# Performance work log

Measured on AMD Instinct MI355X. Metric: run time of the kernel, lower is better.

## Reference

```python
import jax, jax.numpy as jnp
import numpy as np

N_USERS = 50000
N_ITEMS = 20000
N_EDGES = 1_000_000
N_RATINGS = 5
IN_FEAT = 64
HID_FEAT = 64


def setup_inputs() -> dict:
    key = jax.random.key(0)
    k = jax.random.split(key, 6)
    u_s = jax.random.randint(k[0], (N_EDGES,), 0, N_USERS, dtype=jnp.int32)
    v_s = jax.random.randint(k[1], (N_EDGES,), 0, N_ITEMS, dtype=jnp.int32)
    rate = jax.random.randint(k[2], (N_EDGES,), 0, N_RATINGS, dtype=jnp.int32)
    x_user = jax.random.normal(k[3], (N_USERS, IN_FEAT), dtype=jnp.float32)
    x_item = jax.random.normal(k[4], (N_ITEMS, IN_FEAT), dtype=jnp.float32)
    # xavier-uniform with relu gain, as in nn.init.xavier_uniform_(gain=calculate_gain('relu'))
    gain = float(np.sqrt(2.0))
    bound = gain * float(np.sqrt(6.0 / (IN_FEAT + HID_FEAT)))
    weight = jax.random.uniform(k[5], (N_RATINGS, IN_FEAT, HID_FEAT),
                                minval=-bound, maxval=bound, dtype=jnp.float32)
    return {"u_s": u_s, "v_s": v_s, "rate": rate,
            "x_user": x_user, "x_item": x_item, "weight": weight}


def _aggregate(dst, src_feat, rate, n_dst, weight):
    # c_ij in the original = #edges sharing (dst node, rating); so the
    # sum over edges of (x[src] @ W[rate]) / c_ij equals a per-(dst, rating)
    # MEAN of source features followed by the rating-specific matmul.
    seg = dst * N_RATINGS + rate                      # [E] combined segment id
    cnt = jax.ops.segment_sum(jnp.ones_like(src_feat[:, 0]), seg,
                              num_segments=n_dst * N_RATINGS)  # [n_dst*R]
    ssum = jax.ops.segment_sum(src_feat, seg,
                               num_segments=n_dst * N_RATINGS)  # [n_dst*R, in]
    mean = ssum / jnp.maximum(cnt, 1.0)[:, None]
    mean = mean.reshape(n_dst, N_RATINGS, src_feat.shape[1])  # [n_dst, R, in]
    return jnp.einsum('nrd,rdh->nh', mean, weight)            # [n_dst, hid]


def reference(u_s, v_s, rate, x_user, x_item, weight):
    # w_sharing=False -> use weight directly; activation=None; dropout=0 -> identity
    h_u = _aggregate(u_s, x_item[v_s], rate, N_USERS, weight)
    h_v = _aggregate(v_s, x_user[u_s], rate, N_ITEMS, weight)
    return h_u, h_v
```

## Files before the change

kernel.cpp:

```cpp
#include <hip/hip_runtime.h>
#include <hip/hip_bf16.h>

constexpr int N_USERS = 50000;
constexpr int N_ITEMS = 20000;
constexpr int RATES   = 5;
constexpr int F       = 64;

constexpr int N_TOTAL  = N_USERS + N_ITEMS;
constexpr long OUT_FLOATS = (long)N_TOTAL * F;

constexpr int NFB_U = (N_USERS + 31) / 32;
constexpr int NFB_V = (N_ITEMS + 31) / 32;
constexpr int NFBK  = NFB_U + NFB_V;
constexpr int NBKP  = 2304;

constexpr int EPB  = 2048;

constexpr int SLOT = 2048;
constexpr int GCAP = SLOT;

constexpr int SMSTR = 328;

constexpr int LW_TOT = RATES * 8 * 512;

constexpr int TU8 = N_USERS * 8;
constexpr int TI8 = N_ITEMS * 8;
constexpr int TW8 = RATES * 8 * 64;
constexpr int TPREP = TU8 + TI8 + TW8;

typedef short bfrag __attribute__((ext_vector_type(8)));
typedef float vf4   __attribute__((ext_vector_type(4)));

static __device__ __forceinline__ unsigned short f2bf(float f) {
    __hip_bfloat16 h = __float2bfloat16(f);
    return *reinterpret_cast<unsigned short*>(&h);
}

__global__ void zero_ints(int* __restrict__ p, long n) {
    long i = (long)blockIdx.x * blockDim.x + threadIdx.x;
    long stride = (long)gridDim.x * blockDim.x;
    for (long k = i; k < n; k += stride) p[k] = 0;
}

__global__ __launch_bounds__(256) void prep_kernel(
        const float* __restrict__ Xu, const float* __restrict__ Xi,
        const float* __restrict__ W,
        unsigned short* __restrict__ Xbu, unsigned short* __restrict__ Xbi,
        unsigned short* __restrict__ LWg, int* __restrict__ bcursor) {
    int gid = blockIdx.x * 256 + threadIdx.x;
    int stride = gridDim.x * 256;
    for (int i = gid; i < NFBK; i += stride) bcursor[i] = 0;
    for (int t = gid; t < TPREP; t += stride) {
        if (t < TU8 + TI8) {
            const float* src;
            unsigned short* dst;
            if (t < TU8) { src = Xu + (long)t * 8;         dst = Xbu + (long)t * 8; }
            else         { src = Xi + (long)(t - TU8) * 8; dst = Xbi + (long)(t - TU8) * 8; }
            float4 a = *(const float4*)src;
            float4 b = *(const float4*)(src + 4);
            union { bfrag v; unsigned short s[8]; } o;
            o.s[0] = f2bf(a.x); o.s[1] = f2bf(a.y);
            o.s[2] = f2bf(a.z); o.s[3] = f2bf(a.w);
            o.s[4] = f2bf(b.x); o.s[5] = f2bf(b.y);
            o.s[6] = f2bf(b.z); o.s[7] = f2bf(b.w);
            *(bfrag*)dst = o.v;
        } else {
            int t2 = t - TU8 - TI8;
            int r   = t2 >> 9;
            int u   = t2 & 511;
            int kfq = u >> 6;
            int h   = u & 63;
            int kf  = kfq >> 2, q = kfq & 3;
            union { bfrag v; unsigned short s[8]; } o;
#pragma unroll
            for (int j = 0; j < 8; j++)
                o.s[j] = f2bf(W[(r * 64 + kf * 32 + q * 8 + j) * 64 + h]);
            *(bfrag*)&LWg[(((r * 2 + kf) * 4 + q) * 64 + h) * 8] = o.v;
        }
    }
}

__global__ __launch_bounds__(256) void part_kernel(
        const int* __restrict__ u_s, const int* __restrict__ v_s,
        const int* __restrict__ rate,
        int* __restrict__ bcursor, int* __restrict__ sorted_pk, int n_edges) {
    __shared__ int lcnt[NBKP];
    __shared__ int lcur[NBKP];

    int tid = threadIdx.x;
    int e0 = blockIdx.x * EPB;
    int eEnd = min(e0 + EPB, n_edges);

    for (int i = tid; i < NBKP; i += 256) lcnt[i] = 0;
    __syncthreads();
    for (int e = e0 + tid; e < eEnd; e += 256) {
        atomicAdd(&lcnt[u_s[e] >> 5], 1);
        atomicAdd(&lcnt[NFB_U + (v_s[e] >> 5)], 1);
    }
    __syncthreads();
    for (int bb = tid; bb < NFBK; bb += 256) {
        int c = lcnt[bb];
        lcur[bb] = c ? atomicAdd(&bcursor[bb], c) : 0;
    }
    __syncthreads();
    for (int e = e0 + tid; e < eEnd; e += 256) {
        int u = u_s[e], v = v_s[e], r = rate[e];
        int bu = u >> 5;
        int pu = atomicAdd(&lcur[bu], 1);
        if (pu < SLOT)
            sorted_pk[(long)bu * SLOT + pu] = v | (r << 16) | ((u & 31) << 19);
        int bv = NFB_U + (v >> 5);
        int pv = atomicAdd(&lcur[bv], 1);
        if (pv < SLOT)
            sorted_pk[(long)bv * SLOT + pv] = u | (r << 16) | ((v & 31) << 19);
    }
}

__global__ __launch_bounds__(256) void gather_mfma_kernel(
        const int* __restrict__ sorted_pk,
        const int* __restrict__ bcursor,
        const unsigned short* __restrict__ Xbu,
        const unsigned short* __restrict__ Xbi,
        const unsigned short* __restrict__ LWg,
        float* __restrict__ out) {
    __shared__ int perm[GCAP];
    __shared__ int lcnt[32 * RATES];
    __shared__ int lcur[32 * RATES];
    __shared__ float sinvc[32 * RATES];
    __shared__ unsigned short smean[32][SMSTR];
    int* tsum = perm;

    int tid = threadIdx.x, lane = tid & 63, wid = tid >> 6;

    int b = blockIdx.x;
    const unsigned short* Xb;
    float* o;
    int fb, node0, n_nodes;
    if (b < NFB_V) {
        fb = NFB_U + b; node0 = b * 32; n_nodes = N_ITEMS;
        Xb = Xbu; o = out + (long)N_USERS * F;
    } else {
        fb = b - NFB_V; node0 = fb * 32; n_nodes = N_USERS;
        Xb = Xbi; o = out;
    }
    int nn = min(32, n_nodes - node0);
    int nseg = nn * RATES;

    int cnt = min(bcursor[fb], SLOT);
    const int* pkbase = sorted_pk + (long)fb * SLOT;

    int rpk[8];
#pragma unroll
    for (int kk = 0; kk < 8; kk++) {
        int j = kk * 256 + tid;
        rpk[kk] = (j < cnt) ? pkbase[j] : -1;
    }

    for (int i = tid; i < nseg; i += 256) lcnt[i] = 0;
    __syncthreads();
#pragma unroll
    for (int kk = 0; kk < 8; kk++) {
        int pk = rpk[kk];
        if (pk >= 0)
            atomicAdd(&lcnt[((pk >> 19) & 31) * RATES + ((pk >> 16) & 7)], 1);
    }
    __syncthreads();
    int v = (tid < nseg) ? lcnt[tid] : 0;
    tsum[tid] = v;
    __syncthreads();
    for (int off = 1; off < 256; off <<= 1) {
        int x = (tid >= off) ? tsum[tid - off] : 0;
        __syncthreads();
        tsum[tid] += x;
        __syncthreads();
    }
    int excl = tsum[tid] - v;
    if (tid < nseg) {
        lcur[tid]  = excl;
        sinvc[tid] = 1.0f / fmaxf((float)v, 1.0f);
    }
    __syncthreads();
#pragma unroll
    for (int kk = 0; kk < 8; kk++) {
        int pk = rpk[kk];
        if (pk >= 0) {
            int p = atomicAdd(&lcur[((pk >> 19) & 31) * RATES + ((pk >> 16) & 7)], 1);
            if (p < GCAP) perm[p] = pk;
        }
    }
    __syncthreads();

    int g = lane >> 3, ci = lane & 7;
    const unsigned short* xp = Xb + ci * 8;
    for (int oct = wid; oct * 8 < nseg; oct += 4) {
        int sg = oct * 8 + g;
        int S = 0, E = 0;
        if (sg < nseg) {
            S = (sg == 0) ? 0 : min(lcur[sg - 1], GCAP);
            E = min(lcur[sg], GCAP);
        }
        float acc[8];
#pragma unroll
        for (int k = 0; k < 8; k++) acc[k] = 0.f;
        for (int t = S; t < E; t++) {
            int src = perm[t] & 0xFFFF;
            const uint4 y4 = *(const uint4*)(xp + (long)src * F);
            unsigned uu[4] = {y4.x, y4.y, y4.z, y4.w};
#pragma unroll
            for (int qq = 0; qq < 4; qq++) {
                acc[2 * qq]     += __uint_as_float(uu[qq] << 16);
                acc[2 * qq + 1] += __uint_as_float(uu[qq] & 0xffff0000u);
            }
        }
        if (sg < nseg) {
            float sc = sinvc[sg];
            int n = sg / RATES;
            int r = sg - n * RATES;
            union { bfrag v8; unsigned short us[8]; } mv;
#pragma unroll
            for (int k = 0; k < 8; k++) mv.us[k] = f2bf(acc[k] * sc);
            *(bfrag*)&smean[n][r * F + ci * 8] = mv.v8;
        }
    }
    __syncthreads();

    int m = lane & 15, q = lane >> 4;
    int tile = wid & 1, ht0 = wid >> 1;
    if (tile * 16 < nn) {
        const unsigned short* smrow = &smean[tile * 16 + m][0];
        vf4 acc0 = {0.f, 0.f, 0.f, 0.f};
        vf4 acc1 = {0.f, 0.f, 0.f, 0.f};
#pragma unroll
        for (int r = 0; r < RATES; r++) {
            bfrag a0 = *(const bfrag*)(smrow + r * F + q * 8);
            bfrag a1 = *(const bfrag*)(smrow + r * F + 32 + q * 8);
            {
                int h = ht0 * 16 + m;
                bfrag b0 = *(const bfrag*)(LWg + ((r * 2 + 0) * 4 + q) * 512 + h * 8);
                bfrag b1 = *(const bfrag*)(LWg + ((r * 2 + 1) * 4 + q) * 512 + h * 8);
                acc0 = __builtin_amdgcn_mfma_f32_16x16x32_bf16(a0, b0, acc0, 0, 0, 0);
                acc0 = __builtin_amdgcn_mfma_f32_16x16x32_bf16(a1, b1, acc0, 0, 0, 0);
            }
            {
                int h = (ht0 + 2) * 16 + m;
                bfrag b0 = *(const bfrag*)(LWg + ((r * 2 + 0) * 4 + q) * 512 + h * 8);
                bfrag b1 = *(const bfrag*)(LWg + ((r * 2 + 1) * 4 + q) * 512 + h * 8);
                acc1 = __builtin_amdgcn_mfma_f32_16x16x32_bf16(a0, b0, acc1, 0, 0, 0);
                acc1 = __builtin_amdgcn_mfma_f32_16x16x32_bf16(a1, b1, acc1, 0, 0, 0);
            }
        }
        float* obase = o + (long)(node0 + tile * 16 + q * 4) * F;
#pragma unroll
        for (int reg = 0; reg < 4; reg++) {
            obase[(long)reg * F + ht0 * 16 + m]       = acc0[reg];
            obase[(long)reg * F + (ht0 + 2) * 16 + m] = acc1[reg];
        }
    }
}

extern "C" void kernel_launch(void* const* d_in, const int* in_sizes, int n_in,
                              void* d_out, int out_size, void* d_ws, size_t ws_size,
                              hipStream_t stream) {
    const int*   u_s    = (const int*)d_in[0];
    const int*   v_s    = (const int*)d_in[1];
    const int*   rate   = (const int*)d_in[2];
    const float* x_user = (const float*)d_in[3];
    const float* x_item = (const float*)d_in[4];
    const float* W      = (const float*)d_in[5];
    float* out = (float*)d_out;

    int n_edges = in_sizes[0];

    unsigned short* Xbu = (unsigned short*)d_ws;
    unsigned short* Xbi = Xbu + (long)N_USERS * F;
    unsigned short* LWg = Xbi + (long)N_ITEMS * F;
    int* bcursor      = (int*)(LWg + LW_TOT);
    int* sorted_pk    = bcursor + NFBK;
    size_t need = (size_t)((char*)(sorted_pk + (long)NFBK * SLOT) - (char*)d_ws);
    if (need > ws_size) {
        zero_ints<<<2048, 256, 0, stream>>>((int*)out, OUT_FLOATS);
        return;
    }

    prep_kernel<<<(TPREP + 255) / 256, 256, 0, stream>>>(
        x_user, x_item, W, Xbu, Xbi, LWg, bcursor);

    part_kernel<<<(n_edges + EPB - 1) / EPB, 256, 0, stream>>>(
        u_s, v_s, rate, bcursor, sorted_pk, n_edges);

    gather_mfma_kernel<<<NFBK, 256, 0, stream>>>(
        sorted_pk, bcursor, Xbu, Xbi, LWg, out);
}
```

Before: 174.4 us.

## Fuse prep and partition kernels, shuffle-based scan, unrolled gather, smaller perm

```diff
diff --git a/kernel.cpp b/kernel.cpp
--- a/kernel.cpp
+++ b/kernel.cpp
@@ -14,7 +14,7 @@
 constexpr int NFBK  = NFB_U + NFB_V;
 constexpr int NBKP  = 2304;
 
-constexpr int EPB  = 2048;
+constexpr int EPB  = 4096;
 
 constexpr int SLOT = 2048;
 constexpr int GCAP = SLOT;
@@ -27,6 +27,7 @@
 constexpr int TI8 = N_ITEMS * 8;
 constexpr int TW8 = RATES * 8 * 64;
 constexpr int TPREP = TU8 + TI8 + TW8;
+constexpr int GPREP = (TPREP + 255) / 256;
 
 typedef short bfrag __attribute__((ext_vector_type(8)));
 typedef float vf4   __attribute__((ext_vector_type(4)));
@@ -34,6 +35,15 @@
 static __device__ __forceinline__ unsigned short f2bf(float f) {
     __hip_bfloat16 h = __float2bfloat16(f);
     return *reinterpret_cast<unsigned short*>(&h);
+}
+
+static __device__ __forceinline__ void accum8(float* acc, uint4 y) {
+    unsigned uu[4] = {y.x, y.y, y.z, y.w};
+#pragma unroll
+    for (int qq = 0; qq < 4; qq++) {
+        acc[2 * qq]     += __uint_as_float(uu[qq] << 16);
+        acc[2 * qq + 1] += __uint_as_float(uu[qq] & 0xffff0000u);
+    }
 }
 
 __global__ void zero_ints(int* __restrict__ p, long n) {
@@ -42,93 +52,93 @@
     for (long k = i; k < n; k += stride) p[k] = 0;
 }
 
-__global__ __launch_bounds__(256) void prep_kernel(
+__global__ __launch_bounds__(256) void fused_pp_kernel(
+        const int* __restrict__ u_s, const int* __restrict__ v_s,
+        const int* __restrict__ rate,
         const float* __restrict__ Xu, const float* __restrict__ Xi,
         const float* __restrict__ W,
         unsigned short* __restrict__ Xbu, unsigned short* __restrict__ Xbi,
-        unsigned short* __restrict__ LWg, int* __restrict__ bcursor) {
-    int gid = blockIdx.x * 256 + threadIdx.x;
-    int stride = gridDim.x * 256;
-    for (int i = gid; i < NFBK; i += stride) bcursor[i] = 0;
-    for (int t = gid; t < TPREP; t += stride) {
-        if (t < TU8 + TI8) {
-            const float* src;
-            unsigned short* dst;
-            if (t < TU8) { src = Xu + (long)t * 8;         dst = Xbu + (long)t * 8; }
-            else         { src = Xi + (long)(t - TU8) * 8; dst = Xbi + (long)(t - TU8) * 8; }
-            float4 a = *(const float4*)src;
-            float4 b = *(const float4*)(src + 4);
-            union { bfrag v; unsigned short s[8]; } o;
-            o.s[0] = f2bf(a.x); o.s[1] = f2bf(a.y);
-            o.s[2] = f2bf(a.z); o.s[3] = f2bf(a.w);
-            o.s[4] = f2bf(b.x); o.s[5] = f2bf(b.y);
-            o.s[6] = f2bf(b.z); o.s[7] = f2bf(b.w);
-            *(bfrag*)dst = o.v;
-        } else {
-            int t2 = t - TU8 - TI8;
-            int r   = t2 >> 9;
-            int u   = t2 & 511;
-            int kfq = u >> 6;
-            int h   = u & 63;
-            int kf  = kfq >> 2, q = kfq & 3;
-            union { bfrag v; unsigned short s[8]; } o;
-#pragma unroll
-            for (int j = 0; j < 8; j++)
-                o.s[j] = f2bf(W[(r * 64 + kf * 32 + q * 8 + j) * 64 + h]);
-            *(bfrag*)&LWg[(((r * 2 + kf) * 4 + q) * 64 + h) * 8] = o.v;
-        }
-    }
-}
-
-__global__ __launch_bounds__(256) void part_kernel(
-        const int* __restrict__ u_s, const int* __restrict__ v_s,
-        const int* __restrict__ rate,
-        int* __restrict__ bcursor, int* __restrict__ sorted_pk, int n_edges) {
-    __shared__ int lcnt[NBKP];
-    __shared__ int lcur[NBKP];
-
+        unsigned short* __restrict__ LWg,
+        int* __restrict__ bcursor, int* __restrict__ sorted_pk,
+        int n_edges, int npart) {
+    __shared__ int sh[2 * NBKP];
     int tid = threadIdx.x;
-    int e0 = blockIdx.x * EPB;
-    int eEnd = min(e0 + EPB, n_edges);
-
-    for (int i = tid; i < NBKP; i += 256) lcnt[i] = 0;
-    __syncthreads();
-    for (int e = e0 + tid; e < eEnd; e += 256) {
-        atomicAdd(&lcnt[u_s[e] >> 5], 1);
-        atomicAdd(&lcnt[NFB_U + (v_s[e] >> 5)], 1);
-    }
-    __syncthreads();
-    for (int bb = tid; bb < NFBK; bb += 256) {
-        int c = lcnt[bb];
-        lcur[bb] = c ? atomicAdd(&bcursor[bb], c) : 0;
-    }
-    __syncthreads();
-    for (int e = e0 + tid; e < eEnd; e += 256) {
-        int u = u_s[e], v = v_s[e], r = rate[e];
-        int bu = u >> 5;
-        int pu = atomicAdd(&lcur[bu], 1);
-        if (pu < SLOT)
-            sorted_pk[(long)bu * SLOT + pu] = v | (r << 16) | ((u & 31) << 19);
-        int bv = NFB_U + (v >> 5);
-        int pv = atomicAdd(&lcur[bv], 1);
-        if (pv < SLOT)
-            sorted_pk[(long)bv * SLOT + pv] = u | (r << 16) | ((v & 31) << 19);
-    }
-}
-
-__global__ __launch_bounds__(256) void gather_mfma_kernel(
+
+    if ((int)blockIdx.x < npart) {
+        int* lcnt = sh;
+        int* lcur = sh + NBKP;
+        int e0 = blockIdx.x * EPB;
+        int eEnd = min(e0 + EPB, n_edges);
+
+        for (int i = tid; i < NBKP; i += 256) lcnt[i] = 0;
+        __syncthreads();
+        for (int e = e0 + tid; e < eEnd; e += 256) {
+            atomicAdd(&lcnt[u_s[e] >> 5], 1);
+            atomicAdd(&lcnt[NFB_U + (v_s[e] >> 5)], 1);
+        }
+        __syncthreads();
+        for (int bb = tid; bb < NFBK; bb += 256) {
+            int c = lcnt[bb];
+            lcur[bb] = c ? atomicAdd(&bcursor[bb], c) : 0;
+        }
+        __syncthreads();
+        for (int e = e0 + tid; e < eEnd; e += 256) {
+            int u = u_s[e], v = v_s[e], r = rate[e];
+            int bu = u >> 5;
+            int pu = atomicAdd(&lcur[bu], 1);
+            if (pu < SLOT)
+                sorted_pk[(long)bu * SLOT + pu] = v | (r << 16) | ((u & 31) << 19);
+            int bv = NFB_U + (v >> 5);
+            int pv = atomicAdd(&lcur[bv], 1);
+            if (pv < SLOT)
+                sorted_pk[(long)bv * SLOT + pv] = u | (r << 16) | ((v & 31) << 19);
+        }
+    } else {
+        int t = ((int)blockIdx.x - npart) * 256 + tid;
+        if (t < TPREP) {
+            if (t < TU8 + TI8) {
+                const float* src;
+                unsigned short* dst;
+                if (t < TU8) { src = Xu + (long)t * 8;         dst = Xbu + (long)t * 8; }
+                else         { src = Xi + (long)(t - TU8) * 8; dst = Xbi + (long)(t - TU8) * 8; }
+                float4 a = *(const float4*)src;
+                float4 b = *(const float4*)(src + 4);
+                union { bfrag v; unsigned short s[8]; } o;
+                o.s[0] = f2bf(a.x); o.s[1] = f2bf(a.y);
+                o.s[2] = f2bf(a.z); o.s[3] = f2bf(a.w);
+                o.s[4] = f2bf(b.x); o.s[5] = f2bf(b.y);
+                o.s[6] = f2bf(b.z); o.s[7] = f2bf(b.w);
+                *(bfrag*)dst = o.v;
+            } else {
+                int t2 = t - TU8 - TI8;
+                int r   = t2 >> 9;
+                int u   = t2 & 511;
+                int kfq = u >> 6;
+                int h   = u & 63;
+                int kf  = kfq >> 2, q = kfq & 3;
+                union { bfrag v; unsigned short s[8]; } o;
+#pragma unroll
+                for (int j = 0; j < 8; j++)
+                    o.s[j] = f2bf(W[(r * 64 + kf * 32 + q * 8 + j) * 64 + h]);
+                *(bfrag*)&LWg[(((r * 2 + kf) * 4 + q) * 64 + h) * 8] = o.v;
+            }
+        }
+    }
+}
+
+__global__ __launch_bounds__(256, 6) void gather_mfma_kernel(
         const int* __restrict__ sorted_pk,
         const int* __restrict__ bcursor,
         const unsigned short* __restrict__ Xbu,
         const unsigned short* __restrict__ Xbi,
         const unsigned short* __restrict__ LWg,
         float* __restrict__ out) {
-    __shared__ int perm[GCAP];
+    __shared__ unsigned short perm[GCAP];
     __shared__ int lcnt[32 * RATES];
     __shared__ int lcur[32 * RATES];
     __shared__ float sinvc[32 * RATES];
+    __shared__ int wsum[4];
     __shared__ unsigned short smean[32][SMSTR];
-    int* tsum = perm;
 
     int tid = threadIdx.x, lane = tid & 63, wid = tid >> 6;
 
@@ -156,7 +166,7 @@
         rpk[kk] = (j < cnt) ? pkbase[j] : -1;
     }
 
-    for (int i = tid; i < nseg; i += 256) lcnt[i] = 0;
+    if (tid < nseg) lcnt[tid] = 0;
     __syncthreads();
 #pragma unroll
     for (int kk = 0; kk < 8; kk++) {
@@ -165,27 +175,30 @@
             atomicAdd(&lcnt[((pk >> 19) & 31) * RATES + ((pk >> 16) & 7)], 1);
     }
     __syncthreads();
-    int v = (tid < nseg) ? lcnt[tid] : 0;
-    tsum[tid] = v;
-    __syncthreads();
-    for (int off = 1; off < 256; off <<= 1) {
-        int x = (tid >= off) ? tsum[tid - off] : 0;
-        __syncthreads();
-        tsum[tid] += x;
-        __syncthreads();
-    }
-    int excl = tsum[tid] - v;
+
+    int sv = (tid < nseg) ? lcnt[tid] : 0;
+    int inc = sv;
+#pragma unroll
+    for (int off = 1; off < 64; off <<= 1) {
+        int x = __shfl_up(inc, off, 64);
+        if (lane >= off) inc += x;
+    }
+    if (lane == 63 && wid < 3) wsum[wid] = inc;
+    __syncthreads();
+    int prefix = ((wid >= 1) ? wsum[0] : 0) + ((wid >= 2) ? wsum[1] : 0);
+    int excl = prefix + inc - sv;
     if (tid < nseg) {
         lcur[tid]  = excl;
-        sinvc[tid] = 1.0f / fmaxf((float)v, 1.0f);
-    }
-    __syncthreads();
+        sinvc[tid] = 1.0f / fmaxf((float)sv, 1.0f);
+    }
+    __syncthreads();
+
 #pragma unroll
     for (int kk = 0; kk < 8; kk++) {
         int pk = rpk[kk];
         if (pk >= 0) {
             int p = atomicAdd(&lcur[((pk >> 19) & 31) * RATES + ((pk >> 16) & 7)], 1);
-            if (p < GCAP) perm[p] = pk;
+            if (p < GCAP) perm[p] = (unsigned short)(pk & 0xFFFF);
         }
     }
     __syncthreads();
@@ -194,25 +207,28 @@
     const unsigned short* xp = Xb + ci * 8;
     for (int oct = wid; oct * 8 < nseg; oct += 4) {
         int sg = oct * 8 + g;
-        int S = 0, E = 0;
-        if (sg < nseg) {
-            S = (sg == 0) ? 0 : min(lcur[sg - 1], GCAP);
-            E = min(lcur[sg], GCAP);
-        }
+        bool act = sg < nseg;
+        int S = act ? ((sg == 0) ? 0 : min(lcur[sg - 1], GCAP)) : 0;
+        int E = act ? min(lcur[sg], GCAP) : 0;
         float acc[8];
 #pragma unroll
         for (int k = 0; k < 8; k++) acc[k] = 0.f;
-        for (int t = S; t < E; t++) {
-            int src = perm[t] & 0xFFFF;
-            const uint4 y4 = *(const uint4*)(xp + (long)src * F);
-            unsigned uu[4] = {y4.x, y4.y, y4.z, y4.w};
-#pragma unroll
-            for (int qq = 0; qq < 4; qq++) {
-                acc[2 * qq]     += __uint_as_float(uu[qq] << 16);
-                acc[2 * qq + 1] += __uint_as_float(uu[qq] & 0xffff0000u);
-            }
-        }
-        if (sg < nseg) {
+        int t = S;
+        for (; t + 4 <= E; t += 4) {
+            int s0 = perm[t], s1 = perm[t + 1];
+            int s2 = perm[t + 2], s3 = perm[t + 3];
+            uint4 y0 = *(const uint4*)(xp + (long)s0 * F);
+            uint4 y1 = *(const uint4*)(xp + (long)s1 * F);
+            uint4 y2 = *(const uint4*)(xp + (long)s2 * F);
+            uint4 y3 = *(const uint4*)(xp + (long)s3 * F);
+            accum8(acc, y0); accum8(acc, y1);
+            accum8(acc, y2); accum8(acc, y3);
+        }
+        for (; t < E; t++) {
+            int s0 = perm[t];
+            accum8(acc, *(const uint4*)(xp + (long)s0 * F));
+        }
+        if (act) {
             float sc = sinvc[sg];
             int n = sg / RATES;
             int r = sg - n * RATES;
@@ -270,6 +286,7 @@
     float* out = (float*)d_out;
 
     int n_edges = in_sizes[0];
+    int npart = (n_edges + EPB - 1) / EPB;
 
     unsigned short* Xbu = (unsigned short*)d_ws;
     unsigned short* Xbi = Xbu + (long)N_USERS * F;
@@ -282,11 +299,11 @@
         return;
     }
 
-    prep_kernel<<<(TPREP + 255) / 256, 256, 0, stream>>>(
-        x_user, x_item, W, Xbu, Xbi, LWg, bcursor);
-
-    part_kernel<<<(n_edges + EPB - 1) / EPB, 256, 0, stream>>>(
-        u_s, v_s, rate, bcursor, sorted_pk, n_edges);
+    zero_ints<<<1, 256, 0, stream>>>(bcursor, NFBK);
+
+    fused_pp_kernel<<<npart + GPREP, 256, 0, stream>>>(
+        u_s, v_s, rate, x_user, x_item, W,
+        Xbu, Xbi, LWg, bcursor, sorted_pk, n_edges, npart);
 
     gather_mfma_kernel<<<NFBK, 256, 0, stream>>>(
         sorted_pk, bcursor, Xbu, Xbi, LWg, out);
```

New measurement: 159.3 us. 8.6% less time.
